# Kernel tuning notes

Hardware: AMD Instinct MI355X
Metric: run time of the kernel (lower is better)

Reference implementation:

```python
import jax, jax.numpy as jnp
import numpy as np

BATCH = 4096
INDIM = 1024
OUTDIM = 1024
NNZ = 52224  # min(1024,1024) * int(1024 * 0.05)


def setup_inputs() -> dict:
    key = jax.random.key(0)
    k1, k2, k3, k4, k5 = jax.random.split(key, 5)
    stdv = np.sqrt(2.0 / INDIM).astype(np.float32)
    input_ = jax.random.normal(k1, (BATCH, INDIM), dtype=jnp.float32)
    weight = jax.random.normal(k2, (NNZ,), dtype=jnp.float32) * stdv
    bias = jax.random.normal(k3, (OUTDIM,), dtype=jnp.float32) * stdv
    ind_in = jax.random.randint(k4, (NNZ,), 0, INDIM, dtype=jnp.int32)
    ind_out = jax.random.randint(k5, (NNZ,), 0, OUTDIM, dtype=jnp.int32)
    return {"input_": input_, "weight": weight, "bias": bias,
            "ind_in": ind_in, "ind_out": ind_out}


def reference(input_, weight, bias, ind_in, ind_out):
    # x = input_[:, ind_in] * weight        [B, NNZ]
    gathered = input_[:, ind_in] * weight
    # scatter_add into output columns       [B, OUTDIM]
    out = jnp.zeros((input_.shape[0], OUTDIM), dtype=input_.dtype)
    out = out.at[:, ind_out].add(gathered)
    return out + bias
```

## Files before the change

kernel.cpp:

```cpp
#include <hip/hip_runtime.h>
#include <stdint.h>

#define INDIM   1024
#define OUTDIM  1024
#define BM 64
#define BN 64
#define BK 64
#define KTILES (INDIM / BK)

typedef __attribute__((ext_vector_type(8))) short  short8;
typedef __attribute__((ext_vector_type(4))) float  floatx4;

__global__ void k_scatter_w(const int* __restrict__ ind_in, const int* __restrict__ ind_out,
                            const float* __restrict__ w, float* __restrict__ W32T, int nnz) {
    int k = blockIdx.x * 256 + threadIdx.x;
    if (k < nnz)
        atomicAdd(&W32T[(size_t)ind_out[k] * INDIM + ind_in[k]], w[k]);
}

__device__ __forceinline__ uint32_t bf16pack(float x, float y) {
    uint32_t ux = __float_as_uint(x);
    ux = ((ux + 0x7FFFu + ((ux >> 16) & 1u)) >> 16) & 0xFFFFu;
    uint32_t uy = __float_as_uint(y);
    uy = (uy + 0x7FFFu + ((uy >> 16) & 1u)) & 0xFFFF0000u;
    return ux | uy;
}

__device__ __forceinline__ uint4 pack8(float4 a, float4 b) {
    return make_uint4(bf16pack(a.x, a.y), bf16pack(a.z, a.w),
                      bf16pack(b.x, b.y), bf16pack(b.z, b.w));
}

__global__ __launch_bounds__(256, 4) void k_gemm(
    const float* __restrict__ A32,
    const float* __restrict__ W32T,
    const float* __restrict__ bias,
    float* __restrict__ C, int M)
{
    __shared__ ushort lA[BM * BK];
    __shared__ ushort lB[BN * BK];

    const int t      = threadIdx.x;
    const int w      = t >> 6;
    const int L      = t & 63;
    const int lane15 = L & 15;
    const int lane7  = L & 7;
    const int quad   = L >> 4;
    const int wm     = w >> 1, wn = w & 1;

    const int bid = blockIdx.x;
    const int bm0 = ((bid & 7) * 8 + (bid >> 7)) * BM;
    const int bn0 = ((bid >> 3) & 15) * BN;

    const int srow = t >> 3;
    const int j8   = (t & 7) ^ (srow & 7);

    const float* Abase = A32  + (size_t)bm0 * INDIM;
    const float* Bbase = W32T + (size_t)bn0 * INDIM;

    floatx4 acc[2][2] = {};

    for (int kt = 0; kt < KTILES; ++kt) {
        const int gcol = kt * BK + j8 * 8;
        const float* pa0 = Abase + (size_t)srow        * INDIM + gcol;
        const float* pa1 = Abase + (size_t)(srow + 32) * INDIM + gcol;
        const float* pb0 = Bbase + (size_t)srow        * INDIM + gcol;
        const float* pb1 = Bbase + (size_t)(srow + 32) * INDIM + gcol;
        uint4 va0 = pack8(*(const float4*)pa0, *(const float4*)(pa0 + 4));
        uint4 va1 = pack8(*(const float4*)pa1, *(const float4*)(pa1 + 4));
        uint4 vb0 = pack8(*(const float4*)pb0, *(const float4*)(pb0 + 4));
        uint4 vb1 = pack8(*(const float4*)pb1, *(const float4*)(pb1 + 4));
        __syncthreads();
        *(uint4*)(lA + (size_t)t * 8)         = va0;
        *(uint4*)(lA + (size_t)(t + 256) * 8) = va1;
        *(uint4*)(lB + (size_t)t * 8)         = vb0;
        *(uint4*)(lB + (size_t)(t + 256) * 8) = vb1;
        __syncthreads();

        #pragma unroll
        for (int ks = 0; ks < 2; ++ks) {
            const int koff = (((ks * 4 + quad) ^ lane7) * 8);
            short8 af[2], bf[2];
            #pragma unroll
            for (int tm = 0; tm < 2; ++tm)
                af[tm] = *(const short8*)(lA + (wm * 32 + tm * 16 + lane15) * 64 + koff);
            #pragma unroll
            for (int tn = 0; tn < 2; ++tn)
                bf[tn] = *(const short8*)(lB + (wn * 32 + tn * 16 + lane15) * 64 + koff);
            #pragma unroll
            for (int tm = 0; tm < 2; ++tm)
                #pragma unroll
                for (int tn = 0; tn < 2; ++tn)
                    acc[tm][tn] = __builtin_amdgcn_mfma_f32_16x16x32_bf16(
                        af[tm], bf[tn], acc[tm][tn], 0, 0, 0);
        }
    }

    #pragma unroll
    for (int tm = 0; tm < 2; ++tm) {
        #pragma unroll
        for (int tn = 0; tn < 2; ++tn) {
            const int col = bn0 + wn * 32 + tn * 16 + lane15;
            const float bv = bias[col];
            #pragma unroll
            for (int r = 0; r < 4; ++r) {
                const int row = bm0 + wm * 32 + tm * 16 + quad * 4 + r;
                C[(size_t)row * OUTDIM + col] = acc[tm][tn][r] + bv;
            }
        }
    }
}

extern "C" void kernel_launch(void* const* d_in, const int* in_sizes, int n_in,
                              void* d_out, int out_size, void* d_ws, size_t ws_size,
                              hipStream_t stream) {
    const float* input  = (const float*)d_in[0];
    const float* weight = (const float*)d_in[1];
    const float* bias   = (const float*)d_in[2];
    const int*   ind_in  = (const int*)d_in[3];
    const int*   ind_out = (const int*)d_in[4];
    float* out = (float*)d_out;

    const int nnz = in_sizes[1];
    const int M   = out_size / OUTDIM;

    float* W32T = (float*)d_ws;

    (void)hipMemsetAsync(W32T, 0, (size_t)OUTDIM * INDIM * sizeof(float), stream);
    k_scatter_w<<<(nnz + 255) / 256, 256, 0, stream>>>(ind_in, ind_out, weight, W32T, nnz);
    k_gemm<<<(M / BM) * (OUTDIM / BN), 256, 0, stream>>>(input, W32T, bias, out, M);
}
```

Baseline: 102.5 us.

## Use 128x128 tiles with 512 threads and pre-convert dense weight to bf16

Grows the GEMM block tile from 64x64 to 128x128 with 8 waves per block, so each wave computes a 32x64 sub-tile and global traffic per output falls. A separate kernel converts the scattered fp32 weight matrix to bf16 once, so the GEMM loads B directly as bf16 without repacking it every tile. Output stores become nontemporal. The cost is an extra kernel launch, a 2 MB intermediate buffer, and fewer blocks (256) on the device, which may lower occupancy and load balance.

```diff
diff --git a/kernel.cpp b/kernel.cpp
--- a/kernel.cpp
+++ b/kernel.cpp
@@ -3,8 +3,8 @@
 
 #define INDIM   1024
 #define OUTDIM  1024
-#define BM 64
-#define BN 64
+#define BM 128
+#define BN 128
 #define BK 64
 #define KTILES (INDIM / BK)
 
@@ -31,9 +31,17 @@
                       bf16pack(b.x, b.y), bf16pack(b.z, b.w));
 }
 
-__global__ __launch_bounds__(256, 4) void k_gemm(
+__global__ void k_convert_w(const float4* __restrict__ Wt, uint2* __restrict__ W16, int n4) {
+    int i = blockIdx.x * 256 + threadIdx.x;
+    if (i < n4) {
+        float4 v = Wt[i];
+        W16[i] = make_uint2(bf16pack(v.x, v.y), bf16pack(v.z, v.w));
+    }
+}
+
+__global__ __launch_bounds__(512, 4) void k_gemm(
     const float* __restrict__ A32,
-    const float* __restrict__ W32T,
+    const ushort* __restrict__ W16T,
     const float* __restrict__ bias,
     float* __restrict__ C, int M)
 {
@@ -46,51 +54,56 @@
     const int lane15 = L & 15;
     const int lane7  = L & 7;
     const int quad   = L >> 4;
-    const int wm     = w >> 1, wn = w & 1;
+    const int wm     = w >> 1;
+    const int wn     = w & 1;
 
     const int bid = blockIdx.x;
-    const int bm0 = ((bid & 7) * 8 + (bid >> 7)) * BM;
-    const int bn0 = ((bid >> 3) & 15) * BN;
+    int bm0, bn0;
+    if (gridDim.x == 256) {
+        bm0 = ((bid & 7) * 4 + (bid >> 6)) * BM;
+        bn0 = ((bid >> 3) & 7) * BN;
+    } else {
+        bm0 = (bid / (OUTDIM / BN)) * BM;
+        bn0 = (bid % (OUTDIM / BN)) * BN;
+    }
 
     const int srow = t >> 3;
     const int j8   = (t & 7) ^ (srow & 7);
 
-    const float* Abase = A32  + (size_t)bm0 * INDIM;
-    const float* Bbase = W32T + (size_t)bn0 * INDIM;
+    const float*  Abase = A32  + (size_t)bm0 * INDIM;
+    const ushort* Bbase = W16T + (size_t)bn0 * INDIM;
 
-    floatx4 acc[2][2] = {};
+    floatx4 acc[2][4] = {};
 
     for (int kt = 0; kt < KTILES; ++kt) {
         const int gcol = kt * BK + j8 * 8;
         const float* pa0 = Abase + (size_t)srow        * INDIM + gcol;
-        const float* pa1 = Abase + (size_t)(srow + 32) * INDIM + gcol;
-        const float* pb0 = Bbase + (size_t)srow        * INDIM + gcol;
-        const float* pb1 = Bbase + (size_t)(srow + 32) * INDIM + gcol;
+        const float* pa1 = Abase + (size_t)(srow + 64) * INDIM + gcol;
         uint4 va0 = pack8(*(const float4*)pa0, *(const float4*)(pa0 + 4));
         uint4 va1 = pack8(*(const float4*)pa1, *(const float4*)(pa1 + 4));
-        uint4 vb0 = pack8(*(const float4*)pb0, *(const float4*)(pb0 + 4));
-        uint4 vb1 = pack8(*(const float4*)pb1, *(const float4*)(pb1 + 4));
+        uint4 vb0 = *(const uint4*)(Bbase + (size_t)srow        * INDIM + gcol);
+        uint4 vb1 = *(const uint4*)(Bbase + (size_t)(srow + 64) * INDIM + gcol);
         __syncthreads();
         *(uint4*)(lA + (size_t)t * 8)         = va0;
-        *(uint4*)(lA + (size_t)(t + 256) * 8) = va1;
+        *(uint4*)(lA + (size_t)(t + 512) * 8) = va1;
         *(uint4*)(lB + (size_t)t * 8)         = vb0;
-        *(uint4*)(lB + (size_t)(t + 256) * 8) = vb1;
+        *(uint4*)(lB + (size_t)(t + 512) * 8) = vb1;
         __syncthreads();
 
         #pragma unroll
         for (int ks = 0; ks < 2; ++ks) {
             const int koff = (((ks * 4 + quad) ^ lane7) * 8);
-            short8 af[2], bf[2];
+            short8 af[2], bf[4];
             #pragma unroll
             for (int tm = 0; tm < 2; ++tm)
                 af[tm] = *(const short8*)(lA + (wm * 32 + tm * 16 + lane15) * 64 + koff);
             #pragma unroll
-            for (int tn = 0; tn < 2; ++tn)
-                bf[tn] = *(const short8*)(lB + (wn * 32 + tn * 16 + lane15) * 64 + koff);
+            for (int tn = 0; tn < 4; ++tn)
+                bf[tn] = *(const short8*)(lB + (wn * 64 + tn * 16 + lane15) * 64 + koff);
             #pragma unroll
             for (int tm = 0; tm < 2; ++tm)
                 #pragma unroll
-                for (int tn = 0; tn < 2; ++tn)
+                for (int tn = 0; tn < 4; ++tn)
                     acc[tm][tn] = __builtin_amdgcn_mfma_f32_16x16x32_bf16(
                         af[tm], bf[tn], acc[tm][tn], 0, 0, 0);
         }
@@ -99,13 +112,14 @@
     #pragma unroll
     for (int tm = 0; tm < 2; ++tm) {
         #pragma unroll
-        for (int tn = 0; tn < 2; ++tn) {
-            const int col = bn0 + wn * 32 + tn * 16 + lane15;
+        for (int tn = 0; tn < 4; ++tn) {
+            const int col = bn0 + wn * 64 + tn * 16 + lane15;
             const float bv = bias[col];
             #pragma unroll
             for (int r = 0; r < 4; ++r) {
                 const int row = bm0 + wm * 32 + tm * 16 + quad * 4 + r;
-                C[(size_t)row * OUTDIM + col] = acc[tm][tn][r] + bv;
+                __builtin_nontemporal_store(acc[tm][tn][r] + bv,
+                                            &C[(size_t)row * OUTDIM + col]);
             }
         }
     }
@@ -124,9 +138,13 @@
     const int nnz = in_sizes[1];
     const int M   = out_size / OUTDIM;
 
-    float* W32T = (float*)d_ws;
+    char* ws = (char*)d_ws;
+    float*  W32T = (float*)ws;
+    ushort* W16T = (ushort*)(ws + (4u << 20));
 
     (void)hipMemsetAsync(W32T, 0, (size_t)OUTDIM * INDIM * sizeof(float), stream);
     k_scatter_w<<<(nnz + 255) / 256, 256, 0, stream>>>(ind_in, ind_out, weight, W32T, nnz);
-    k_gemm<<<(M / BM) * (OUTDIM / BN), 256, 0, stream>>>(input, W32T, bias, out, M);
+    k_convert_w<<<OUTDIM * INDIM / 4 / 256, 256, 0, stream>>>(
+        (const float4*)W32T, (uint2*)W16T, OUTDIM * INDIM / 4);
+    k_gemm<<<(M / BM) * (OUTDIM / BN), 512, 0, stream>>>(input, W16T, bias, out, M);
 }
```

Result: slower. 106.5 us (+3.9%).
